# Kernel optimization log

Hardware: AMD Instinct MI355X
Metric: run time of the kernel (lower is better)

Reference implementation:

```python
import jax, jax.numpy as jnp
import numpy as np

FILTER_SIZE = 5
C_IN = 32
C_OUT = 64
N = 8192


def setup_inputs() -> dict:
    key = jax.random.key(0)
    k1, k2, k3 = jax.random.split(key, 3)
    L = jax.random.normal(k1, (N, N), dtype=jnp.float32) / np.float32(np.sqrt(N))
    x = jax.random.normal(k2, (C_IN, N), dtype=jnp.float32)
    theta = jax.random.normal(k3, (C_OUT, C_IN, FILTER_SIZE), dtype=jnp.float32)  # variance=1.0
    bias = jnp.zeros((C_OUT, 1), dtype=jnp.float32)
    return {"L": L, "x": x, "theta": theta, "bias": bias}


def reference(L, x, theta, bias):
    # Chebyshev recurrence vectorized over all input channels at once.
    # Original does per-channel column matvecs L @ x[c]; here T_k has shape
    # (C_in, N) and L @ x_col per channel == T @ L.T.
    T_prev = x                      # T_0, (C_in, N)
    Ts = [T_prev]
    if FILTER_SIZE > 1:
        T_curr = T_prev @ L.T       # T_1
        Ts.append(T_curr)
        for _ in range(2, FILTER_SIZE):
            T_next = 2.0 * (T_curr @ L.T) - T_prev
            Ts.append(T_next)
            T_prev, T_curr = T_curr, T_next
    X = jnp.stack(Ts, axis=-1)      # (C_in, N, K) — matches torch assemble
    y = jnp.einsum('imk,oik->om', X, theta) + bias  # (C_out, N)
    return y
```

## Files before the change

### kernel.cpp

```cpp
#include <hip/hip_runtime.h>

#define NN 8192
#define CIN 32
#define COUT 64
#define KF 5

typedef __attribute__((ext_vector_type(8))) short bf16x8_t;
typedef __attribute__((ext_vector_type(4))) float f32x4_t;

__device__ __forceinline__ short f2bf(float f) {
    unsigned u = __builtin_bit_cast(unsigned, f);
    unsigned r = (u + 0x7FFFu + ((u >> 16) & 1u)) >> 16;
    return (short)(unsigned short)r;
}

__device__ __forceinline__ bf16x8_t cvt8(float4 a, float4 b) {
    bf16x8_t v;
    v[0] = f2bf(a.x); v[1] = f2bf(a.y); v[2] = f2bf(a.z); v[3] = f2bf(a.w);
    v[4] = f2bf(b.x); v[5] = f2bf(b.y); v[6] = f2bf(b.z); v[7] = f2bf(b.w);
    return v;
}

__global__ void cvt_kernel(const float* __restrict__ src, short* __restrict__ dst) {
    int idx = blockIdx.x * 256 + threadIdx.x;
    float4 v = reinterpret_cast<const float4*>(src)[idx];
    short4 o;
    o.x = f2bf(v.x); o.y = f2bf(v.y); o.z = f2bf(v.z); o.w = f2bf(v.w);
    reinterpret_cast<short4*>(dst)[idx] = o;
}

__device__ __forceinline__ void stash_partials(float* red, int wave, int g, int r,
                                               const f32x4_t& acc0, const f32x4_t& acc1) {
    const int base = wave * 512 + g * 64 + r;
#pragma unroll
    for (int t = 0; t < 4; ++t) {
        red[base + t * 16]       = acc0[t];
        red[base + t * 16 + 256] = acc1[t];
    }
}

__device__ __forceinline__ void reduce_write(const float* red, int tid, int i0,
                                             float alpha, const float* __restrict__ Tprev,
                                             float* __restrict__ Tf, short* __restrict__ Tb) {
    __syncthreads();
    const int c = tid >> 4, il = tid & 15;
    float s = red[tid];
#pragma unroll
    for (int w = 1; w < 8; ++w) s += red[w * 512 + tid];
    float val = alpha * s;
    const size_t off = (size_t)c * NN + i0 + il;
    if (Tprev) val -= Tprev[off];
    Tf[off] = val;
    Tb[off] = f2bf(val);
}

__device__ __forceinline__ void mfma_range(const short* __restrict__ Lb,
                                           const short* __restrict__ A,
                                           int i0, int r, int g, int jb,
                                           f32x4_t& acc0, f32x4_t& acc1) {
    const short* Lrow = Lb + (size_t)(i0 + r) * NN;
    for (int j = jb; j < jb + NN / 8; j += 32) {
        const int jl = j + g * 8;
        bf16x8_t b  = *reinterpret_cast<const bf16x8_t*>(Lrow + jl);
        bf16x8_t a0 = *reinterpret_cast<const bf16x8_t*>(A + (size_t)r * NN + jl);
        bf16x8_t a1 = *reinterpret_cast<const bf16x8_t*>(A + (size_t)(r + 16) * NN + jl);
        acc0 = __builtin_amdgcn_mfma_f32_16x16x32_bf16(a0, b, acc0, 0, 0, 0);
        acc1 = __builtin_amdgcn_mfma_f32_16x16x32_bf16(a1, b, acc1, 0, 0, 0);
    }
}

__global__ __launch_bounds__(512, 4) void pass1_kernel(
    const float* __restrict__ L, const short* __restrict__ Tb0,
    short* __restrict__ Lb, float* __restrict__ Tf1, short* __restrict__ Tb1)
{
    __shared__ float red[8 * 512];
    const int tid = threadIdx.x, wave = tid >> 6, lane = tid & 63;
    const int g = lane >> 4, r = lane & 15;
    const int i0 = blockIdx.x * 16;
    const int jb = wave * (NN / 8);

    const float* Lrow = L + (size_t)(i0 + r) * NN;
    short* LbRow = Lb + (size_t)(i0 + r) * NN;
    f32x4_t acc0 = {0.f, 0.f, 0.f, 0.f};
    f32x4_t acc1 = {0.f, 0.f, 0.f, 0.f};
    for (int j = jb; j < jb + NN / 8; j += 32) {
        const int jl = j + g * 8;
        float4 l0 = *reinterpret_cast<const float4*>(Lrow + jl);
        float4 l1 = *reinterpret_cast<const float4*>(Lrow + jl + 4);
        bf16x8_t b = cvt8(l0, l1);
        *reinterpret_cast<bf16x8_t*>(LbRow + jl) = b;
        bf16x8_t a0 = *reinterpret_cast<const bf16x8_t*>(Tb0 + (size_t)r * NN + jl);
        bf16x8_t a1 = *reinterpret_cast<const bf16x8_t*>(Tb0 + (size_t)(r + 16) * NN + jl);
        acc0 = __builtin_amdgcn_mfma_f32_16x16x32_bf16(a0, b, acc0, 0, 0, 0);
        acc1 = __builtin_amdgcn_mfma_f32_16x16x32_bf16(a1, b, acc1, 0, 0, 0);
    }
    stash_partials(red, wave, g, r, acc0, acc1);
    reduce_write(red, tid, i0, 1.0f, nullptr, Tf1, Tb1);
}

__global__ __launch_bounds__(512, 4) void passmid_kernel(
    const short* __restrict__ Lb, const short* __restrict__ Tbin,
    const float* __restrict__ Tprev, float* __restrict__ Tf, short* __restrict__ Tb)
{
    __shared__ float red[8 * 512];
    const int tid = threadIdx.x, wave = tid >> 6, lane = tid & 63;
    const int g = lane >> 4, r = lane & 15;
    const int i0 = blockIdx.x * 16;
    f32x4_t acc0 = {0.f, 0.f, 0.f, 0.f};
    f32x4_t acc1 = {0.f, 0.f, 0.f, 0.f};
    mfma_range(Lb, Tbin, i0, r, g, wave * (NN / 8), acc0, acc1);
    stash_partials(red, wave, g, r, acc0, acc1);
    reduce_write(red, tid, i0, 2.0f, Tprev, Tf, Tb);
}

__global__ __launch_bounds__(512, 4) void pass4_kernel(
    const short* __restrict__ Lb, const short* __restrict__ Tb3,
    const float* __restrict__ Tf2, const float* __restrict__ x,
    const float* __restrict__ Tf1, const float* __restrict__ Tf3,
    const float* __restrict__ theta, const float* __restrict__ bias,
    float* __restrict__ y)
{
    __shared__ float red[8 * 512];
    __shared__ float thS[COUT * CIN * KF];
    const int tid = threadIdx.x, wave = tid >> 6, lane = tid & 63;
    const int g = lane >> 4, r = lane & 15;
    const int i0 = blockIdx.x * 16;
    f32x4_t acc0 = {0.f, 0.f, 0.f, 0.f};
    f32x4_t acc1 = {0.f, 0.f, 0.f, 0.f};
    mfma_range(Lb, Tb3, i0, r, g, wave * (NN / 8), acc0, acc1);
    stash_partials(red, wave, g, r, acc0, acc1);
    __syncthreads();

    {
        const int c = tid >> 4, il = tid & 15;
        float s = red[tid];
#pragma unroll
        for (int w = 1; w < 8; ++w) s += red[w * 512 + tid];
        red[tid] = 2.0f * s - Tf2[(size_t)c * NN + i0 + il];
    }
    for (int t = tid; t < COUT * CIN * KF; t += 512) thS[t] = theta[t];
    __syncthreads();

    const int o0 = tid >> 4, il = tid & 15;
    float a0 = bias[o0], a1 = bias[o0 + 32];
    for (int c = 0; c < CIN; ++c) {
        const size_t off = (size_t)c * NN + i0 + il;
        const float t0 = x[off], t1 = Tf1[off], t2 = Tf2[off], t3 = Tf3[off];
        const float t4 = red[c * 16 + il];
        const float* th0 = &thS[(o0 * CIN + c) * KF];
        const float* th1 = &thS[((o0 + 32) * CIN + c) * KF];
        a0 += t0 * th0[0] + t1 * th0[1] + t2 * th0[2] + t3 * th0[3] + t4 * th0[4];
        a1 += t0 * th1[0] + t1 * th1[1] + t2 * th1[2] + t3 * th1[3] + t4 * th1[4];
    }
    y[(size_t)o0 * NN + i0 + il]        = a0;
    y[(size_t)(o0 + 32) * NN + i0 + il] = a1;
}

extern "C" void kernel_launch(void* const* d_in, const int* in_sizes, int n_in,
                              void* d_out, int out_size, void* d_ws, size_t ws_size,
                              hipStream_t stream) {
    const float* L     = (const float*)d_in[0];
    const float* x     = (const float*)d_in[1];
    const float* theta = (const float*)d_in[2];
    const float* bias  = (const float*)d_in[3];
    float* y = (float*)d_out;

    const size_t TE = (size_t)CIN * NN;
    const size_t LE = (size_t)NN * NN;

    short* Lb  = (short*)d_ws;
    float* Tf1 = (float*)(Lb + LE);
    float* Tf2 = Tf1 + TE;
    float* Tf3 = Tf2 + TE;
    short* Tb0 = (short*)(Tf3 + TE);
    short* Tb1 = Tb0 + TE;
    short* Tb2 = Tb1 + TE;
    short* Tb3 = Tb2 + TE;

    cvt_kernel<<<256, 256, 0, stream>>>(x, Tb0);
    pass1_kernel<<<NN / 16, 512, 0, stream>>>(L, Tb0, Lb, Tf1, Tb1);
    passmid_kernel<<<NN / 16, 512, 0, stream>>>(Lb, Tb1, x,   Tf2, Tb2);
    passmid_kernel<<<NN / 16, 512, 0, stream>>>(Lb, Tb2, Tf1, Tf3, Tb3);
    pass4_kernel<<<NN / 16, 512, 0, stream>>>(Lb, Tb3, Tf2, x, Tf1, Tf3, theta, bias, y);
}
```

Measured before the change: 265.1 us.

## Split-K the L matvec passes into halves with separate combine and output kernels

Each middle Chebyshev pass now splits the reduction over N into two halves, doubling the block count to 1024. Each block writes a partial sum, and a small elementwise combine kernel applies 2*sum - Tprev and produces the fp32 and bf16 copies. The last pass no longer does the theta projection inline. A separate final kernel reads theta from global memory and computes two output channels per thread. The goal is more parallelism and occupancy for the bandwidth-bound L streaming, at the cost of extra launches and partial-buffer round trips.

```diff
diff --git a/kernel.cpp b/kernel.cpp
--- a/kernel.cpp
+++ b/kernel.cpp
@@ -39,34 +39,11 @@
     }
 }
 
-__device__ __forceinline__ void reduce_write(const float* red, int tid, int i0,
-                                             float alpha, const float* __restrict__ Tprev,
-                                             float* __restrict__ Tf, short* __restrict__ Tb) {
-    __syncthreads();
-    const int c = tid >> 4, il = tid & 15;
+__device__ __forceinline__ float reduce8(const float* red, int tid) {
     float s = red[tid];
 #pragma unroll
     for (int w = 1; w < 8; ++w) s += red[w * 512 + tid];
-    float val = alpha * s;
-    const size_t off = (size_t)c * NN + i0 + il;
-    if (Tprev) val -= Tprev[off];
-    Tf[off] = val;
-    Tb[off] = f2bf(val);
-}
-
-__device__ __forceinline__ void mfma_range(const short* __restrict__ Lb,
-                                           const short* __restrict__ A,
-                                           int i0, int r, int g, int jb,
-                                           f32x4_t& acc0, f32x4_t& acc1) {
-    const short* Lrow = Lb + (size_t)(i0 + r) * NN;
-    for (int j = jb; j < jb + NN / 8; j += 32) {
-        const int jl = j + g * 8;
-        bf16x8_t b  = *reinterpret_cast<const bf16x8_t*>(Lrow + jl);
-        bf16x8_t a0 = *reinterpret_cast<const bf16x8_t*>(A + (size_t)r * NN + jl);
-        bf16x8_t a1 = *reinterpret_cast<const bf16x8_t*>(A + (size_t)(r + 16) * NN + jl);
-        acc0 = __builtin_amdgcn_mfma_f32_16x16x32_bf16(a0, b, acc0, 0, 0, 0);
-        acc1 = __builtin_amdgcn_mfma_f32_16x16x32_bf16(a1, b, acc1, 0, 0, 0);
-    }
+    return s;
 }
 
 __global__ __launch_bounds__(512, 4) void pass1_kernel(
@@ -95,65 +72,89 @@
         acc1 = __builtin_amdgcn_mfma_f32_16x16x32_bf16(a1, b, acc1, 0, 0, 0);
     }
     stash_partials(red, wave, g, r, acc0, acc1);
-    reduce_write(red, tid, i0, 1.0f, nullptr, Tf1, Tb1);
+    __syncthreads();
+    const int c = tid >> 4, il = tid & 15;
+    const float val = reduce8(red, tid);
+    const size_t off = (size_t)c * NN + i0 + il;
+    Tf1[off] = val;
+    Tb1[off] = f2bf(val);
 }
 
-__global__ __launch_bounds__(512, 4) void passmid_kernel(
-    const short* __restrict__ Lb, const short* __restrict__ Tbin,
-    const float* __restrict__ Tprev, float* __restrict__ Tf, short* __restrict__ Tb)
+__global__ __launch_bounds__(512, 8) void passmid_kernel(
+    const short* __restrict__ Lb, const short* __restrict__ A,
+    float* __restrict__ part)
 {
     __shared__ float red[8 * 512];
     const int tid = threadIdx.x, wave = tid >> 6, lane = tid & 63;
     const int g = lane >> 4, r = lane & 15;
-    const int i0 = blockIdx.x * 16;
+    const int t = blockIdx.x >> 1, h = blockIdx.x & 1;
+    const int i0 = t * 16;
+    const int jb = h * 4096 + wave * 512;
+
+    const short* Lrow = Lb + (size_t)(i0 + r) * NN;
+    const short* A0 = A + (size_t)r * NN;
+    const short* A1 = A + (size_t)(r + 16) * NN;
+
     f32x4_t acc0 = {0.f, 0.f, 0.f, 0.f};
     f32x4_t acc1 = {0.f, 0.f, 0.f, 0.f};
-    mfma_range(Lb, Tbin, i0, r, g, wave * (NN / 8), acc0, acc1);
+#pragma unroll 4
+    for (int it = 0; it < 16; ++it) {
+        const int jl = jb + it * 32 + g * 8;
+        bf16x8_t b  = *reinterpret_cast<const bf16x8_t*>(Lrow + jl);
+        bf16x8_t a0 = *reinterpret_cast<const bf16x8_t*>(A0 + jl);
+        bf16x8_t a1 = *reinterpret_cast<const bf16x8_t*>(A1 + jl);
+        acc0 = __builtin_amdgcn_mfma_f32_16x16x32_bf16(a0, b, acc0, 0, 0, 0);
+        acc1 = __builtin_amdgcn_mfma_f32_16x16x32_bf16(a1, b, acc1, 0, 0, 0);
+    }
+
     stash_partials(red, wave, g, r, acc0, acc1);
-    reduce_write(red, tid, i0, 2.0f, Tprev, Tf, Tb);
+    __syncthreads();
+    const int c = tid >> 4, il = tid & 15;
+    part[(size_t)h * CIN * NN + (size_t)c * NN + i0 + il] = reduce8(red, tid);
 }
 
-__global__ __launch_bounds__(512, 4) void pass4_kernel(
-    const short* __restrict__ Lb, const short* __restrict__ Tb3,
-    const float* __restrict__ Tf2, const float* __restrict__ x,
-    const float* __restrict__ Tf1, const float* __restrict__ Tf3,
+__global__ __launch_bounds__(256) void combine_kernel(
+    const float* __restrict__ part, const float* __restrict__ Tprev,
+    float* __restrict__ Tf, short* __restrict__ Tb)
+{
+    const int idx = blockIdx.x * 256 + threadIdx.x;
+    const float4 p0 = reinterpret_cast<const float4*>(part)[idx];
+    const float4 p1 = reinterpret_cast<const float4*>(part + (size_t)CIN * NN)[idx];
+    const float4 tp = reinterpret_cast<const float4*>(Tprev)[idx];
+    float4 v;
+    v.x = 2.f * (p0.x + p1.x) - tp.x;
+    v.y = 2.f * (p0.y + p1.y) - tp.y;
+    v.z = 2.f * (p0.z + p1.z) - tp.z;
+    v.w = 2.f * (p0.w + p1.w) - tp.w;
+    reinterpret_cast<float4*>(Tf)[idx] = v;
+    short4 b;
+    b.x = f2bf(v.x); b.y = f2bf(v.y); b.z = f2bf(v.z); b.w = f2bf(v.w);
+    reinterpret_cast<short4*>(Tb)[idx] = b;
+}
+
+__global__ __launch_bounds__(256) void final_kernel(
+    const float* __restrict__ x, const float* __restrict__ Tf1,
+    const float* __restrict__ Tf2, const float* __restrict__ Tf3,
+    const float* __restrict__ part,
     const float* __restrict__ theta, const float* __restrict__ bias,
     float* __restrict__ y)
 {
-    __shared__ float red[8 * 512];
-    __shared__ float thS[COUT * CIN * KF];
-    const int tid = threadIdx.x, wave = tid >> 6, lane = tid & 63;
-    const int g = lane >> 4, r = lane & 15;
-    const int i0 = blockIdx.x * 16;
-    f32x4_t acc0 = {0.f, 0.f, 0.f, 0.f};
-    f32x4_t acc1 = {0.f, 0.f, 0.f, 0.f};
-    mfma_range(Lb, Tb3, i0, r, g, wave * (NN / 8), acc0, acc1);
-    stash_partials(red, wave, g, r, acc0, acc1);
-    __syncthreads();
-
-    {
-        const int c = tid >> 4, il = tid & 15;
-        float s = red[tid];
-#pragma unroll
-        for (int w = 1; w < 8; ++w) s += red[w * 512 + tid];
-        red[tid] = 2.0f * s - Tf2[(size_t)c * NN + i0 + il];
-    }
-    for (int t = tid; t < COUT * CIN * KF; t += 512) thS[t] = theta[t];
-    __syncthreads();
-
-    const int o0 = tid >> 4, il = tid & 15;
-    float a0 = bias[o0], a1 = bias[o0 + 32];
+    const long idx = (long)blockIdx.x * 256 + threadIdx.x;
+    const int i = (int)(idx & (NN - 1));
+    const int op = (int)(idx >> 13);
+    const int o0 = op * 2, o1 = op * 2 + 1;
+    float a0 = bias[o0], a1 = bias[o1];
     for (int c = 0; c < CIN; ++c) {
-        const size_t off = (size_t)c * NN + i0 + il;
+        const size_t off = (size_t)c * NN + i;
         const float t0 = x[off], t1 = Tf1[off], t2 = Tf2[off], t3 = Tf3[off];
-        const float t4 = red[c * 16 + il];
-        const float* th0 = &thS[(o0 * CIN + c) * KF];
-        const float* th1 = &thS[((o0 + 32) * CIN + c) * KF];
+        const float t4 = 2.f * (part[off] + part[(size_t)CIN * NN + off]) - t2;
+        const float* th0 = theta + ((size_t)o0 * CIN + c) * KF;
+        const float* th1 = theta + ((size_t)o1 * CIN + c) * KF;
         a0 += t0 * th0[0] + t1 * th0[1] + t2 * th0[2] + t3 * th0[3] + t4 * th0[4];
         a1 += t0 * th1[0] + t1 * th1[1] + t2 * th1[2] + t3 * th1[3] + t4 * th1[4];
     }
-    y[(size_t)o0 * NN + i0 + il]        = a0;
-    y[(size_t)(o0 + 32) * NN + i0 + il] = a1;
+    y[(size_t)o0 * NN + i] = a0;
+    y[(size_t)o1 * NN + i] = a1;
 }
 
 extern "C" void kernel_launch(void* const* d_in, const int* in_sizes, int n_in,
@@ -176,10 +177,18 @@
     short* Tb1 = Tb0 + TE;
     short* Tb2 = Tb1 + TE;
     short* Tb3 = Tb2 + TE;
+    float* part = (float*)(Tb3 + TE);
 
     cvt_kernel<<<256, 256, 0, stream>>>(x, Tb0);
     pass1_kernel<<<NN / 16, 512, 0, stream>>>(L, Tb0, Lb, Tf1, Tb1);
-    passmid_kernel<<<NN / 16, 512, 0, stream>>>(Lb, Tb1, x,   Tf2, Tb2);
-    passmid_kernel<<<NN / 16, 512, 0, stream>>>(Lb, Tb2, Tf1, Tf3, Tb3);
-    pass4_kernel<<<NN / 16, 512, 0, stream>>>(Lb, Tb3, Tf2, x, Tf1, Tf3, theta, bias, y);
+
+    passmid_kernel<<<NN / 8, 512, 0, stream>>>(Lb, Tb1, part);
+    combine_kernel<<<TE / 4 / 256, 256, 0, stream>>>(part, x, Tf2, Tb2);
+
+    passmid_kernel<<<NN / 8, 512, 0, stream>>>(Lb, Tb2, part);
+    combine_kernel<<<TE / 4 / 256, 256, 0, stream>>>(part, Tf1, Tf3, Tb3);
+
+    passmid_kernel<<<NN / 8, 512, 0, stream>>>(Lb, Tb3, part);
+    final_kernel<<<(COUT / 2) * NN / 256, 256, 0, stream>>>(
+        x, Tf1, Tf2, Tf3, part, theta, bias, y);
 }
```

After: 282.0 us. 6.4% more time.

## Double-buffer L and T operands via global_load_lds async copies in GEMV passes

Applied to the files above, without the earlier changes.

Each wave now streams its slice of L and the bf16 T operands into a private double-buffered LDS stage using global_load_lds, issuing the next chunk's loads before consuming the current one and gating with manual vmcnt/lgkmcnt waits. The aim is to keep more memory requests in flight and hide global-load latency in these bandwidth-bound passes. Pass4 also drops the shared-memory theta copy and reads theta straight from global memory. The extra LDS per block may lower occupancy, and the hand-written waitcnt counts are fragile if the compiler reorders memory operations.

```diff
diff --git a/kernel.cpp b/kernel.cpp
--- a/kernel.cpp
+++ b/kernel.cpp
@@ -19,6 +19,12 @@
     v[0] = f2bf(a.x); v[1] = f2bf(a.y); v[2] = f2bf(a.z); v[3] = f2bf(a.w);
     v[4] = f2bf(b.x); v[5] = f2bf(b.y); v[6] = f2bf(b.z); v[7] = f2bf(b.w);
     return v;
+}
+
+typedef const __attribute__((address_space(1))) void* as1_t;
+typedef __attribute__((address_space(3))) void* as3_t;
+__device__ __forceinline__ void gll16(const void* g, void* l) {
+    __builtin_amdgcn_global_load_lds((as1_t)g, (as3_t)l, 16, 0, 0);
 }
 
 __global__ void cvt_kernel(const float* __restrict__ src, short* __restrict__ dst) {
@@ -39,34 +45,11 @@
     }
 }
 
-__device__ __forceinline__ void reduce_write(const float* red, int tid, int i0,
-                                             float alpha, const float* __restrict__ Tprev,
-                                             float* __restrict__ Tf, short* __restrict__ Tb) {
-    __syncthreads();
-    const int c = tid >> 4, il = tid & 15;
+__device__ __forceinline__ float reduce8(const float* red, int tid) {
     float s = red[tid];
 #pragma unroll
     for (int w = 1; w < 8; ++w) s += red[w * 512 + tid];
-    float val = alpha * s;
-    const size_t off = (size_t)c * NN + i0 + il;
-    if (Tprev) val -= Tprev[off];
-    Tf[off] = val;
-    Tb[off] = f2bf(val);
-}
-
-__device__ __forceinline__ void mfma_range(const short* __restrict__ Lb,
-                                           const short* __restrict__ A,
-                                           int i0, int r, int g, int jb,
-                                           f32x4_t& acc0, f32x4_t& acc1) {
-    const short* Lrow = Lb + (size_t)(i0 + r) * NN;
-    for (int j = jb; j < jb + NN / 8; j += 32) {
-        const int jl = j + g * 8;
-        bf16x8_t b  = *reinterpret_cast<const bf16x8_t*>(Lrow + jl);
-        bf16x8_t a0 = *reinterpret_cast<const bf16x8_t*>(A + (size_t)r * NN + jl);
-        bf16x8_t a1 = *reinterpret_cast<const bf16x8_t*>(A + (size_t)(r + 16) * NN + jl);
-        acc0 = __builtin_amdgcn_mfma_f32_16x16x32_bf16(a0, b, acc0, 0, 0, 0);
-        acc1 = __builtin_amdgcn_mfma_f32_16x16x32_bf16(a1, b, acc1, 0, 0, 0);
-    }
+    return s;
 }
 
 __global__ __launch_bounds__(512, 4) void pass1_kernel(
@@ -74,86 +57,188 @@
     short* __restrict__ Lb, float* __restrict__ Tf1, short* __restrict__ Tb1)
 {
     __shared__ float red[8 * 512];
+    __shared__ __align__(16) char stage[8][8192];
     const int tid = threadIdx.x, wave = tid >> 6, lane = tid & 63;
     const int g = lane >> 4, r = lane & 15;
     const int i0 = blockIdx.x * 16;
-    const int jb = wave * (NN / 8);
-
-    const float* Lrow = L + (size_t)(i0 + r) * NN;
-    short* LbRow = Lb + (size_t)(i0 + r) * NN;
-    f32x4_t acc0 = {0.f, 0.f, 0.f, 0.f};
-    f32x4_t acc1 = {0.f, 0.f, 0.f, 0.f};
-    for (int j = jb; j < jb + NN / 8; j += 32) {
-        const int jl = j + g * 8;
-        float4 l0 = *reinterpret_cast<const float4*>(Lrow + jl);
-        float4 l1 = *reinterpret_cast<const float4*>(Lrow + jl + 4);
+    const int jb = wave * 1024;
+    char* st = stage[wave];
+
+    const float* sL  = L   + (size_t)(i0 + r) * NN + jb + g * 4;
+    const short* sA0 = Tb0 + (size_t)r * NN        + jb + g * 8;
+    const short* sA1 = Tb0 + (size_t)(r + 16) * NN + jb + g * 8;
+    short* dL = Lb + (size_t)(i0 + r) * NN + jb + g * 8;
+
+    const int loL = (g >> 1) * 1024 + (g & 1) * 512 + r * 16;
+    const int lo  = lane * 16;
+
+    gll16(sL,       st + 0);
+    gll16(sL + 16,  st + 1024);
+    gll16(sA0,      st + 4096);
+    gll16(sA1,      st + 5120);
+    gll16(sL + 32,  st + 2048);
+    gll16(sL + 48,  st + 3072);
+    gll16(sA0 + 32, st + 6144);
+    gll16(sA1 + 32, st + 7168);
+
+    f32x4_t acc0 = {0.f,0.f,0.f,0.f};
+    f32x4_t acc1 = {0.f,0.f,0.f,0.f};
+#pragma unroll 2
+    for (int t = 0; t < 32; ++t) {
+        if (t == 0)      asm volatile("s_waitcnt vmcnt(4)" ::: "memory");
+        else if (t < 31) asm volatile("s_waitcnt vmcnt(5)" ::: "memory");
+        else             asm volatile("s_waitcnt vmcnt(1)" ::: "memory");
+        const int sl = t & 1;
+        float4 l0 = *(const float4*)(st + sl * 2048 + loL);
+        float4 l1 = *(const float4*)(st + sl * 2048 + loL + 256);
+        bf16x8_t a0 = *(const bf16x8_t*)(st + 4096 + sl * 2048 + lo);
+        bf16x8_t a1 = *(const bf16x8_t*)(st + 4096 + sl * 2048 + 1024 + lo);
         bf16x8_t b = cvt8(l0, l1);
-        *reinterpret_cast<bf16x8_t*>(LbRow + jl) = b;
-        bf16x8_t a0 = *reinterpret_cast<const bf16x8_t*>(Tb0 + (size_t)r * NN + jl);
-        bf16x8_t a1 = *reinterpret_cast<const bf16x8_t*>(Tb0 + (size_t)(r + 16) * NN + jl);
+        *(bf16x8_t*)(dL + t * 32) = b;
         acc0 = __builtin_amdgcn_mfma_f32_16x16x32_bf16(a0, b, acc0, 0, 0, 0);
         acc1 = __builtin_amdgcn_mfma_f32_16x16x32_bf16(a1, b, acc1, 0, 0, 0);
-    }
+        if (t < 30) {
+            const int adv = (t + 2) * 32;
+            asm volatile("s_waitcnt lgkmcnt(0)" ::: "memory");
+            gll16(sL + adv,      st + sl * 2048);
+            gll16(sL + adv + 16, st + sl * 2048 + 1024);
+            gll16(sA0 + adv,     st + 4096 + sl * 2048);
+            gll16(sA1 + adv,     st + 4096 + sl * 2048 + 1024);
+        }
+    }
+
     stash_partials(red, wave, g, r, acc0, acc1);
-    reduce_write(red, tid, i0, 1.0f, nullptr, Tf1, Tb1);
+    __syncthreads();
+    const int c = tid >> 4, il = tid & 15;
+    const float val = reduce8(red, tid);
+    const size_t off = (size_t)c * NN + i0 + il;
+    Tf1[off] = val;
+    Tb1[off] = f2bf(val);
 }
 
 __global__ __launch_bounds__(512, 4) void passmid_kernel(
-    const short* __restrict__ Lb, const short* __restrict__ Tbin,
+    const short* __restrict__ Lbm, const short* __restrict__ A,
     const float* __restrict__ Tprev, float* __restrict__ Tf, short* __restrict__ Tb)
 {
     __shared__ float red[8 * 512];
+    __shared__ __align__(16) char stage[8][6144];
     const int tid = threadIdx.x, wave = tid >> 6, lane = tid & 63;
     const int g = lane >> 4, r = lane & 15;
     const int i0 = blockIdx.x * 16;
-    f32x4_t acc0 = {0.f, 0.f, 0.f, 0.f};
-    f32x4_t acc1 = {0.f, 0.f, 0.f, 0.f};
-    mfma_range(Lb, Tbin, i0, r, g, wave * (NN / 8), acc0, acc1);
+    const int jb = wave * 1024;
+    char* st = stage[wave];
+
+    const short* sL  = Lbm + (size_t)(i0 + r) * NN + jb + g * 8;
+    const short* sA0 = A   + (size_t)r * NN        + jb + g * 8;
+    const short* sA1 = A   + (size_t)(r + 16) * NN + jb + g * 8;
+    const int lo = lane * 16;
+
+    gll16(sL,       st + 0);
+    gll16(sA0,      st + 2048);
+    gll16(sA1,      st + 3072);
+    gll16(sL + 32,  st + 1024);
+    gll16(sA0 + 32, st + 4096);
+    gll16(sA1 + 32, st + 5120);
+
+    f32x4_t acc0 = {0.f,0.f,0.f,0.f};
+    f32x4_t acc1 = {0.f,0.f,0.f,0.f};
+#pragma unroll 2
+    for (int t = 0; t < 32; ++t) {
+        if (t < 31) asm volatile("s_waitcnt vmcnt(3)" ::: "memory");
+        else        asm volatile("s_waitcnt vmcnt(0)" ::: "memory");
+        const int sl = t & 1;
+        bf16x8_t b  = *(const bf16x8_t*)(st + sl * 1024 + lo);
+        bf16x8_t a0 = *(const bf16x8_t*)(st + 2048 + sl * 2048 + lo);
+        bf16x8_t a1 = *(const bf16x8_t*)(st + 2048 + sl * 2048 + 1024 + lo);
+        acc0 = __builtin_amdgcn_mfma_f32_16x16x32_bf16(a0, b, acc0, 0, 0, 0);
+        acc1 = __builtin_amdgcn_mfma_f32_16x16x32_bf16(a1, b, acc1, 0, 0, 0);
+        if (t < 30) {
+            const int adv = (t + 2) * 32;
+            asm volatile("s_waitcnt lgkmcnt(0)" ::: "memory");
+            gll16(sL + adv,  st + sl * 1024);
+            gll16(sA0 + adv, st + 2048 + sl * 2048);
+            gll16(sA1 + adv, st + 2048 + sl * 2048 + 1024);
+        }
+    }
+
     stash_partials(red, wave, g, r, acc0, acc1);
-    reduce_write(red, tid, i0, 2.0f, Tprev, Tf, Tb);
+    __syncthreads();
+    const int c = tid >> 4, il = tid & 15;
+    const size_t off = (size_t)c * NN + i0 + il;
+    const float val = 2.0f * reduce8(red, tid) - Tprev[off];
+    Tf[off] = val;
+    Tb[off] = f2bf(val);
 }
 
 __global__ __launch_bounds__(512, 4) void pass4_kernel(
-    const short* __restrict__ Lb, const short* __restrict__ Tb3,
+    const short* __restrict__ Lbm, const short* __restrict__ A,
     const float* __restrict__ Tf2, const float* __restrict__ x,
     const float* __restrict__ Tf1, const float* __restrict__ Tf3,
     const float* __restrict__ theta, const float* __restrict__ bias,
     float* __restrict__ y)
 {
     __shared__ float red[8 * 512];
-    __shared__ float thS[COUT * CIN * KF];
+    __shared__ __align__(16) char stage[8][6144];
     const int tid = threadIdx.x, wave = tid >> 6, lane = tid & 63;
     const int g = lane >> 4, r = lane & 15;
     const int i0 = blockIdx.x * 16;
-    f32x4_t acc0 = {0.f, 0.f, 0.f, 0.f};
-    f32x4_t acc1 = {0.f, 0.f, 0.f, 0.f};
-    mfma_range(Lb, Tb3, i0, r, g, wave * (NN / 8), acc0, acc1);
+    const int jb = wave * 1024;
+    char* st = stage[wave];
+
+    const short* sL  = Lbm + (size_t)(i0 + r) * NN + jb + g * 8;
+    const short* sA0 = A   + (size_t)r * NN        + jb + g * 8;
+    const short* sA1 = A   + (size_t)(r + 16) * NN + jb + g * 8;
+    const int lo = lane * 16;
+
+    gll16(sL,       st + 0);
+    gll16(sA0,      st + 2048);
+    gll16(sA1,      st + 3072);
+    gll16(sL + 32,  st + 1024);
+    gll16(sA0 + 32, st + 4096);
+    gll16(sA1 + 32, st + 5120);
+
+    f32x4_t acc0 = {0.f,0.f,0.f,0.f};
+    f32x4_t acc1 = {0.f,0.f,0.f,0.f};
+#pragma unroll 2
+    for (int t = 0; t < 32; ++t) {
+        if (t < 31) asm volatile("s_waitcnt vmcnt(3)" ::: "memory");
+        else        asm volatile("s_waitcnt vmcnt(0)" ::: "memory");
+        const int sl = t & 1;
+        bf16x8_t b  = *(const bf16x8_t*)(st + sl * 1024 + lo);
+        bf16x8_t a0 = *(const bf16x8_t*)(st + 2048 + sl * 2048 + lo);
+        bf16x8_t a1 = *(const bf16x8_t*)(st + 2048 + sl * 2048 + 1024 + lo);
+        acc0 = __builtin_amdgcn_mfma_f32_16x16x32_bf16(a0, b, acc0, 0, 0, 0);
+        acc1 = __builtin_amdgcn_mfma_f32_16x16x32_bf16(a1, b, acc1, 0, 0, 0);
+        if (t < 30) {
+            const int adv = (t + 2) * 32;
+            asm volatile("s_waitcnt lgkmcnt(0)" ::: "memory");
+            gll16(sL + adv,  st + sl * 1024);
+            gll16(sA0 + adv, st + 2048 + sl * 2048);
+            gll16(sA1 + adv, st + 2048 + sl * 2048 + 1024);
+        }
+    }
+
     stash_partials(red, wave, g, r, acc0, acc1);
     __syncthreads();
-
     {
         const int c = tid >> 4, il = tid & 15;
-        float s = red[tid];
-#pragma unroll
-        for (int w = 1; w < 8; ++w) s += red[w * 512 + tid];
-        red[tid] = 2.0f * s - Tf2[(size_t)c * NN + i0 + il];
-    }
-    for (int t = tid; t < COUT * CIN * KF; t += 512) thS[t] = theta[t];
-    __syncthreads();
-
-    const int o0 = tid >> 4, il = tid & 15;
-    float a0 = bias[o0], a1 = bias[o0 + 32];
-    for (int c = 0; c < CIN; ++c) {
-        const size_t off = (size_t)c * NN + i0 + il;
+        red[tid] = 2.0f * reduce8(red, tid) - Tf2[(size_t)c * NN + i0 + il];
+    }
+    __syncthreads();
+
+    const int o = tid >> 4, il = tid & 15;
+    float a0 = bias[o], a1 = bias[o + 32];
+    for (int cc = 0; cc < CIN; ++cc) {
+        const size_t off = (size_t)cc * NN + i0 + il;
         const float t0 = x[off], t1 = Tf1[off], t2 = Tf2[off], t3 = Tf3[off];
-        const float t4 = red[c * 16 + il];
-        const float* th0 = &thS[(o0 * CIN + c) * KF];
-        const float* th1 = &thS[((o0 + 32) * CIN + c) * KF];
+        const float t4 = red[cc * 16 + il];
+        const float* th0 = theta + ((size_t)o * CIN + cc) * KF;
+        const float* th1 = theta + ((size_t)(o + 32) * CIN + cc) * KF;
         a0 += t0 * th0[0] + t1 * th0[1] + t2 * th0[2] + t3 * th0[3] + t4 * th0[4];
         a1 += t0 * th1[0] + t1 * th1[1] + t2 * th1[2] + t3 * th1[3] + t4 * th1[4];
     }
-    y[(size_t)o0 * NN + i0 + il]        = a0;
-    y[(size_t)(o0 + 32) * NN + i0 + il] = a1;
+    y[(size_t)o * NN + i0 + il]        = a0;
+    y[(size_t)(o + 32) * NN + i0 + il] = a1;
 }
 
 extern "C" void kernel_launch(void* const* d_in, const int* in_sizes, int n_in,
@@ -181,5 +266,6 @@
     pass1_kernel<<<NN / 16, 512, 0, stream>>>(L, Tb0, Lb, Tf1, Tb1);
     passmid_kernel<<<NN / 16, 512, 0, stream>>>(Lb, Tb1, x,   Tf2, Tb2);
     passmid_kernel<<<NN / 16, 512, 0, stream>>>(Lb, Tb2, Tf1, Tf3, Tb3);
-    pass4_kernel<<<NN / 16, 512, 0, stream>>>(Lb, Tb3, Tf2, x, Tf1, Tf3, theta, bias, y);
-}
+    pass4_kernel<<<NN / 16, 512, 0, stream>>>(Lb, Tb3, Tf2, x, Tf1, Tf3,
+                                              theta, bias, y);
+}
```

Result: slower. 288.1 us (+8.7%).

## Stage L and T tiles via async global-to-LDS loads with pre-swizzled bf16 L layout

Applied to the files above, without the earlier changes.

Replaces the direct global loads in all four matvec passes with double-buffered global_load_lds transfers into per-wave LDS staging, using explicit vmcnt waits to overlap memory with MFMA. Pass 1 now writes the bf16 copy of L in a tiled fragment-ordered layout, so later passes can copy contiguous 1 KB chunks straight into LDS. Theta is read from global instead of being staged in shared memory in the last pass, and occupancy is lowered to 2 blocks per CU to fit the larger LDS use. The goal is to hide memory latency on the bandwidth-bound L streaming, at the cost of lower occupancy and hand-tuned wait counts that are fragile.

```diff
diff --git a/kernel.cpp b/kernel.cpp
--- a/kernel.cpp
+++ b/kernel.cpp
@@ -7,6 +7,12 @@
 
 typedef __attribute__((ext_vector_type(8))) short bf16x8_t;
 typedef __attribute__((ext_vector_type(4))) float f32x4_t;
+
+typedef const __attribute__((address_space(1))) void* as1_t;
+typedef __attribute__((address_space(3))) void* as3_t;
+__device__ __forceinline__ void gll16(const void* g, void* l) {
+    __builtin_amdgcn_global_load_lds((as1_t)g, (as3_t)l, 16, 0, 0);
+}
 
 __device__ __forceinline__ short f2bf(float f) {
     unsigned u = __builtin_bit_cast(unsigned, f);
@@ -39,121 +45,190 @@
     }
 }
 
-__device__ __forceinline__ void reduce_write(const float* red, int tid, int i0,
-                                             float alpha, const float* __restrict__ Tprev,
-                                             float* __restrict__ Tf, short* __restrict__ Tb) {
+__device__ __forceinline__ float reduce8(const float* red, int tid) {
+    float s = red[tid];
+#pragma unroll
+    for (int w = 1; w < 8; ++w) s += red[w * 512 + tid];
+    return s;
+}
+
+__device__ __forceinline__ void mid_core(const char* __restrict__ LbW,
+                                         const short* __restrict__ Abase,
+                                         int wave, int lane, char* stg,
+                                         f32x4_t& acc0, f32x4_t& acc1)
+{
+    const int g = lane >> 4, r = lane & 15;
+    const int kw = wave * 1024;
+    const char* srcL = LbW + lane * 16;
+    const short* sA0 = Abase + (size_t)(lane & 31) * NN + kw + (lane >> 5) * 8;
+
+#pragma unroll
+    for (int c0 = 0; c0 < 2; ++c0) {
+        char* Ld = stg + c0 * 6144;
+        char* Ad = Ld + 2048;
+        gll16(srcL + c0 * 2048,        Ld);
+        gll16(srcL + c0 * 2048 + 1024, Ld + 1024);
+#pragma unroll
+        for (int j = 0; j < 4; ++j) gll16(sA0 + c0 * 64 + j * 16, Ad + j * 1024);
+    }
+
+    for (int c = 0; c < 16; ++c) {
+        if (c < 15) asm volatile("s_waitcnt vmcnt(6)" ::: "memory");
+        else        asm volatile("s_waitcnt vmcnt(0)" ::: "memory");
+        const char* Ld = stg + (c & 1) * 6144;
+        const char* Ad = Ld + 2048;
+#pragma unroll
+        for (int kk = 0; kk < 2; ++kk) {
+            bf16x8_t b  = *(const bf16x8_t*)(Ld + (kk * 4 + g) * 256 + r * 16);
+            bf16x8_t a0 = *(const bf16x8_t*)(Ad + (kk * 4 + g) * 512 + r * 16);
+            bf16x8_t a1 = *(const bf16x8_t*)(Ad + (kk * 4 + g) * 512 + 256 + r * 16);
+            acc0 = __builtin_amdgcn_mfma_f32_16x16x32_bf16(a0, b, acc0, 0, 0, 0);
+            acc1 = __builtin_amdgcn_mfma_f32_16x16x32_bf16(a1, b, acc1, 0, 0, 0);
+        }
+        if (c < 14) {
+            asm volatile("s_waitcnt lgkmcnt(0)" ::: "memory");
+            const int cn = c + 2;
+            char* Ldn = stg + (cn & 1) * 6144;
+            char* Adn = Ldn + 2048;
+            gll16(srcL + cn * 2048,        Ldn);
+            gll16(srcL + cn * 2048 + 1024, Ldn + 1024);
+#pragma unroll
+            for (int j = 0; j < 4; ++j) gll16(sA0 + cn * 64 + j * 16, Adn + j * 1024);
+        }
+    }
+}
+
+__global__ __launch_bounds__(512, 2) void pass1_kernel(
+    const float* __restrict__ L, const short* __restrict__ Tb0,
+    char* __restrict__ LbC, float* __restrict__ Tf1, short* __restrict__ Tb1)
+{
+    __shared__ float red[4096];
+    __shared__ __align__(16) char stg[8][16384];
+    const int tid = threadIdx.x, wave = tid >> 6, lane = tid & 63;
+    const int g = lane >> 4, r = lane & 15;
+    const int t = blockIdx.x, i0 = t * 16;
+    const int kw = wave * 1024;
+    char* st = stg[wave];
+
+    const int ls = lane >> 4, cb = (lane & 15) * 16;
+    const float* baseL[4];
+#pragma unroll
+    for (int j = 0; j < 4; ++j) {
+        const int row = 4 * j + ls;
+        baseL[j] = L + (size_t)(i0 + row) * NN + kw + ((cb ^ ((row & 7) << 4)) >> 2);
+    }
+    const short* sA0 = Tb0 + (size_t)(lane & 31) * NN + kw + (lane >> 5) * 8;
+    char* LbW = LbC + (size_t)t * 262144 + wave * 32768;
+
+#pragma unroll
+    for (int c0 = 0; c0 < 2; ++c0) {
+        char* Ld = st + c0 * 8192;
+        char* Ad = Ld + 4096;
+#pragma unroll
+        for (int j = 0; j < 4; ++j) gll16(baseL[j] + c0 * 64, Ld + j * 1024);
+#pragma unroll
+        for (int j = 0; j < 4; ++j) gll16(sA0 + c0 * 64 + j * 16, Ad + j * 1024);
+    }
+
+    f32x4_t acc0 = {0.f,0.f,0.f,0.f}, acc1 = {0.f,0.f,0.f,0.f};
+    const int Xr = (r & 7) << 4;
+    for (int c = 0; c < 16; ++c) {
+        if (c == 0)      asm volatile("s_waitcnt vmcnt(8)" ::: "memory");
+        else if (c < 15) asm volatile("s_waitcnt vmcnt(10)" ::: "memory");
+        else             asm volatile("s_waitcnt vmcnt(2)" ::: "memory");
+        const char* Ld = st + (c & 1) * 8192;
+        const char* Ad = Ld + 4096;
+#pragma unroll
+        for (int kk = 0; kk < 2; ++kk) {
+            float4 l0 = *(const float4*)(Ld + r * 256 + ((kk * 128 + g * 32) ^ Xr));
+            float4 l1 = *(const float4*)(Ld + r * 256 + ((kk * 128 + g * 32 + 16) ^ Xr));
+            bf16x8_t b = cvt8(l0, l1);
+            *(bf16x8_t*)(LbW + c * 2048 + kk * 1024 + lane * 16) = b;
+            bf16x8_t a0 = *(const bf16x8_t*)(Ad + (kk * 4 + g) * 512 + r * 16);
+            bf16x8_t a1 = *(const bf16x8_t*)(Ad + (kk * 4 + g) * 512 + 256 + r * 16);
+            acc0 = __builtin_amdgcn_mfma_f32_16x16x32_bf16(a0, b, acc0, 0, 0, 0);
+            acc1 = __builtin_amdgcn_mfma_f32_16x16x32_bf16(a1, b, acc1, 0, 0, 0);
+        }
+        if (c < 14) {
+            asm volatile("s_waitcnt lgkmcnt(0)" ::: "memory");
+            const int cn = c + 2;
+            char* Ldn = st + (cn & 1) * 8192;
+            char* Adn = Ldn + 4096;
+#pragma unroll
+            for (int j = 0; j < 4; ++j) gll16(baseL[j] + cn * 64, Ldn + j * 1024);
+#pragma unroll
+            for (int j = 0; j < 4; ++j) gll16(sA0 + cn * 64 + j * 16, Adn + j * 1024);
+        }
+    }
+
+    stash_partials(red, wave, g, r, acc0, acc1);
     __syncthreads();
     const int c = tid >> 4, il = tid & 15;
-    float s = red[tid];
-#pragma unroll
-    for (int w = 1; w < 8; ++w) s += red[w * 512 + tid];
-    float val = alpha * s;
+    const float val = reduce8(red, tid);
     const size_t off = (size_t)c * NN + i0 + il;
-    if (Tprev) val -= Tprev[off];
+    Tf1[off] = val;
+    Tb1[off] = f2bf(val);
+}
+
+__global__ __launch_bounds__(512, 2) void passmid_kernel(
+    const char* __restrict__ LbC, const short* __restrict__ A,
+    const float* __restrict__ Tprev, float* __restrict__ Tf, short* __restrict__ Tb)
+{
+    __shared__ float red[4096];
+    __shared__ __align__(16) char stg[8][12288];
+    const int tid = threadIdx.x, wave = tid >> 6, lane = tid & 63;
+    const int g = lane >> 4, r = lane & 15;
+    const int t = blockIdx.x, i0 = t * 16;
+
+    f32x4_t acc0 = {0.f,0.f,0.f,0.f}, acc1 = {0.f,0.f,0.f,0.f};
+    mid_core(LbC + (size_t)t * 262144 + wave * 32768, A, wave, lane, stg[wave], acc0, acc1);
+
+    stash_partials(red, wave, g, r, acc0, acc1);
+    __syncthreads();
+    const int c = tid >> 4, il = tid & 15;
+    const size_t off = (size_t)c * NN + i0 + il;
+    const float val = 2.0f * reduce8(red, tid) - Tprev[off];
     Tf[off] = val;
     Tb[off] = f2bf(val);
 }
 
-__device__ __forceinline__ void mfma_range(const short* __restrict__ Lb,
-                                           const short* __restrict__ A,
-                                           int i0, int r, int g, int jb,
-                                           f32x4_t& acc0, f32x4_t& acc1) {
-    const short* Lrow = Lb + (size_t)(i0 + r) * NN;
-    for (int j = jb; j < jb + NN / 8; j += 32) {
-        const int jl = j + g * 8;
-        bf16x8_t b  = *reinterpret_cast<const bf16x8_t*>(Lrow + jl);
-        bf16x8_t a0 = *reinterpret_cast<const bf16x8_t*>(A + (size_t)r * NN + jl);
-        bf16x8_t a1 = *reinterpret_cast<const bf16x8_t*>(A + (size_t)(r + 16) * NN + jl);
-        acc0 = __builtin_amdgcn_mfma_f32_16x16x32_bf16(a0, b, acc0, 0, 0, 0);
-        acc1 = __builtin_amdgcn_mfma_f32_16x16x32_bf16(a1, b, acc1, 0, 0, 0);
-    }
-}
-
-__global__ __launch_bounds__(512, 4) void pass1_kernel(
-    const float* __restrict__ L, const short* __restrict__ Tb0,
-    short* __restrict__ Lb, float* __restrict__ Tf1, short* __restrict__ Tb1)
-{
-    __shared__ float red[8 * 512];
-    const int tid = threadIdx.x, wave = tid >> 6, lane = tid & 63;
-    const int g = lane >> 4, r = lane & 15;
-    const int i0 = blockIdx.x * 16;
-    const int jb = wave * (NN / 8);
-
-    const float* Lrow = L + (size_t)(i0 + r) * NN;
-    short* LbRow = Lb + (size_t)(i0 + r) * NN;
-    f32x4_t acc0 = {0.f, 0.f, 0.f, 0.f};
-    f32x4_t acc1 = {0.f, 0.f, 0.f, 0.f};
-    for (int j = jb; j < jb + NN / 8; j += 32) {
-        const int jl = j + g * 8;
-        float4 l0 = *reinterpret_cast<const float4*>(Lrow + jl);
-        float4 l1 = *reinterpret_cast<const float4*>(Lrow + jl + 4);
-        bf16x8_t b = cvt8(l0, l1);
-        *reinterpret_cast<bf16x8_t*>(LbRow + jl) = b;
-        bf16x8_t a0 = *reinterpret_cast<const bf16x8_t*>(Tb0 + (size_t)r * NN + jl);
-        bf16x8_t a1 = *reinterpret_cast<const bf16x8_t*>(Tb0 + (size_t)(r + 16) * NN + jl);
-        acc0 = __builtin_amdgcn_mfma_f32_16x16x32_bf16(a0, b, acc0, 0, 0, 0);
-        acc1 = __builtin_amdgcn_mfma_f32_16x16x32_bf16(a1, b, acc1, 0, 0, 0);
-    }
-    stash_partials(red, wave, g, r, acc0, acc1);
-    reduce_write(red, tid, i0, 1.0f, nullptr, Tf1, Tb1);
-}
-
-__global__ __launch_bounds__(512, 4) void passmid_kernel(
-    const short* __restrict__ Lb, const short* __restrict__ Tbin,
-    const float* __restrict__ Tprev, float* __restrict__ Tf, short* __restrict__ Tb)
-{
-    __shared__ float red[8 * 512];
-    const int tid = threadIdx.x, wave = tid >> 6, lane = tid & 63;
-    const int g = lane >> 4, r = lane & 15;
-    const int i0 = blockIdx.x * 16;
-    f32x4_t acc0 = {0.f, 0.f, 0.f, 0.f};
-    f32x4_t acc1 = {0.f, 0.f, 0.f, 0.f};
-    mfma_range(Lb, Tbin, i0, r, g, wave * (NN / 8), acc0, acc1);
-    stash_partials(red, wave, g, r, acc0, acc1);
-    reduce_write(red, tid, i0, 2.0f, Tprev, Tf, Tb);
-}
-
-__global__ __launch_bounds__(512, 4) void pass4_kernel(
-    const short* __restrict__ Lb, const short* __restrict__ Tb3,
+__global__ __launch_bounds__(512, 2) void pass4_kernel(
+    const char* __restrict__ LbC, const short* __restrict__ A,
     const float* __restrict__ Tf2, const float* __restrict__ x,
     const float* __restrict__ Tf1, const float* __restrict__ Tf3,
     const float* __restrict__ theta, const float* __restrict__ bias,
     float* __restrict__ y)
 {
-    __shared__ float red[8 * 512];
-    __shared__ float thS[COUT * CIN * KF];
+    __shared__ float red[4096];
+    __shared__ __align__(16) char stg[8][12288];
     const int tid = threadIdx.x, wave = tid >> 6, lane = tid & 63;
     const int g = lane >> 4, r = lane & 15;
-    const int i0 = blockIdx.x * 16;
-    f32x4_t acc0 = {0.f, 0.f, 0.f, 0.f};
-    f32x4_t acc1 = {0.f, 0.f, 0.f, 0.f};
-    mfma_range(Lb, Tb3, i0, r, g, wave * (NN / 8), acc0, acc1);
+    const int t = blockIdx.x, i0 = t * 16;
+
+    f32x4_t acc0 = {0.f,0.f,0.f,0.f}, acc1 = {0.f,0.f,0.f,0.f};
+    mid_core(LbC + (size_t)t * 262144 + wave * 32768, A, wave, lane, stg[wave], acc0, acc1);
+
     stash_partials(red, wave, g, r, acc0, acc1);
     __syncthreads();
-
     {
         const int c = tid >> 4, il = tid & 15;
-        float s = red[tid];
-#pragma unroll
-        for (int w = 1; w < 8; ++w) s += red[w * 512 + tid];
-        red[tid] = 2.0f * s - Tf2[(size_t)c * NN + i0 + il];
-    }
-    for (int t = tid; t < COUT * CIN * KF; t += 512) thS[t] = theta[t];
-    __syncthreads();
-
-    const int o0 = tid >> 4, il = tid & 15;
-    float a0 = bias[o0], a1 = bias[o0 + 32];
-    for (int c = 0; c < CIN; ++c) {
-        const size_t off = (size_t)c * NN + i0 + il;
+        red[tid] = 2.0f * reduce8(red, tid) - Tf2[(size_t)c * NN + i0 + il];
+    }
+    __syncthreads();
+
+    const int o = tid >> 4, il = tid & 15;
+    float a0 = bias[o], a1 = bias[o + 32];
+    for (int cc = 0; cc < CIN; ++cc) {
+        const size_t off = (size_t)cc * NN + i0 + il;
         const float t0 = x[off], t1 = Tf1[off], t2 = Tf2[off], t3 = Tf3[off];
-        const float t4 = red[c * 16 + il];
-        const float* th0 = &thS[(o0 * CIN + c) * KF];
-        const float* th1 = &thS[((o0 + 32) * CIN + c) * KF];
+        const float t4 = red[cc * 16 + il];
+        const float* th0 = theta + ((size_t)o * CIN + cc) * KF;
+        const float* th1 = theta + ((size_t)(o + 32) * CIN + cc) * KF;
         a0 += t0 * th0[0] + t1 * th0[1] + t2 * th0[2] + t3 * th0[3] + t4 * th0[4];
         a1 += t0 * th1[0] + t1 * th1[1] + t2 * th1[2] + t3 * th1[3] + t4 * th1[4];
     }
-    y[(size_t)o0 * NN + i0 + il]        = a0;
-    y[(size_t)(o0 + 32) * NN + i0 + il] = a1;
+    y[(size_t)o * NN + i0 + il]        = a0;
+    y[(size_t)(o + 32) * NN + i0 + il] = a1;
 }
 
 extern "C" void kernel_launch(void* const* d_in, const int* in_sizes, int n_in,
@@ -168,8 +243,8 @@
     const size_t TE = (size_t)CIN * NN;
     const size_t LE = (size_t)NN * NN;
 
-    short* Lb  = (short*)d_ws;
-    float* Tf1 = (float*)(Lb + LE);
+    char*  LbC = (char*)d_ws;
+    float* Tf1 = (float*)(LbC + LE * 2);
     float* Tf2 = Tf1 + TE;
     float* Tf3 = Tf2 + TE;
     short* Tb0 = (short*)(Tf3 + TE);
@@ -178,8 +253,9 @@
     short* Tb3 = Tb2 + TE;
 
     cvt_kernel<<<256, 256, 0, stream>>>(x, Tb0);
-    pass1_kernel<<<NN / 16, 512, 0, stream>>>(L, Tb0, Lb, Tf1, Tb1);
-    passmid_kernel<<<NN / 16, 512, 0, stream>>>(Lb, Tb1, x,   Tf2, Tb2);
-    passmid_kernel<<<NN / 16, 512, 0, stream>>>(Lb, Tb2, Tf1, Tf3, Tb3);
-    pass4_kernel<<<NN / 16, 512, 0, stream>>>(Lb, Tb3, Tf2, x, Tf1, Tf3, theta, bias, y);
-}
+    pass1_kernel<<<NN / 16, 512, 0, stream>>>(L, Tb0, LbC, Tf1, Tb1);
+    passmid_kernel<<<NN / 16, 512, 0, stream>>>(LbC, Tb1, x,   Tf2, Tb2);
+    passmid_kernel<<<NN / 16, 512, 0, stream>>>(LbC, Tb2, Tf1, Tf3, Tb3);
+    pass4_kernel<<<NN / 16, 512, 0, stream>>>(LbC, Tb3, Tf2, x, Tf1, Tf3,
+                                              theta, bias, y);
+}
```

Measured after the change: 252.1 us. -4.9%, faster.
